# Performance work log

Hardware: AMD Instinct MI355X
Metric: run time of the kernel (lower is better)

## Reference

```python
import jax, jax.numpy as jnp
import numpy as np

N = 14           # num_wires
DEPTH = 2        # feature_map_depth; circuit applies DEPTH+1 StronglyEntanglingLayers blocks
SEL_LAYERS = 2   # params (B, 2*N*3) -> weights (B, 2, N, 3)


def _apply_1q(psi, U, w):
    # psi: (B, 2**N) complex64, U: (B,2,2) complex64, acts on wire w (wire 0 = MSB)
    B = psi.shape[0]
    psi = psi.reshape(B, 2 ** w, 2, -1)
    psi = jnp.einsum('bij,bajc->baic', U, psi)
    return psi.reshape(B, -1)


def _apply_cnot(psi, c, t):
    B = psi.shape[0]
    x = psi.reshape((B,) + (2,) * N)
    ca, ta = 1 + c, 1 + t
    a0 = jax.lax.index_in_dim(x, 0, ca, keepdims=True)
    a1 = jnp.flip(jax.lax.index_in_dim(x, 1, ca, keepdims=True), axis=ta)
    return jnp.concatenate([a0, a1], axis=ca).reshape(B, -1)


def _expz(psi, w):
    # <Z_w> = P(bit_w = 0) - P(bit_w = 1)
    B = psi.shape[0]
    p = (psi.real ** 2 + psi.imag ** 2).reshape(B, 2 ** w, 2, -1)
    return p[:, :, 0].sum(axis=(1, 2)) - p[:, :, 1].sum(axis=(1, 2))


def _rot(phi, theta, omega):
    # PennyLane Rot = RZ(omega) RY(theta) RZ(phi); returns (B,2,2) complex
    c, s = jnp.cos(theta / 2), jnp.sin(theta / 2)
    u00 = jnp.exp(-0.5j * (phi + omega)) * c
    u01 = -jnp.exp(0.5j * (phi - omega)) * s
    u10 = jnp.exp(-0.5j * (phi - omega)) * s
    u11 = jnp.exp(0.5j * (phi + omega)) * c
    return jnp.stack([jnp.stack([u00, u01], -1), jnp.stack([u10, u11], -1)], -2)


def _circuit(phases, weights):
    # phases: (B, N) float32, weights: (B, SEL_LAYERS, N, 3) float32
    B = phases.shape[0]
    psi = jnp.zeros((B, 2 ** N), jnp.complex64).at[:, 0].set(1.0)
    # AngleEmbedding (rotation='X'): RX(phi_w) on each wire
    for w in range(N):
        th = phases[:, w] / 2
        c, s = jnp.cos(th), jnp.sin(th)
        U = jnp.stack([jnp.stack([c + 0j, -1j * s], -1),
                       jnp.stack([-1j * s, c + 0j], -1)], -2)
        psi = _apply_1q(psi, U.astype(jnp.complex64), w)
    # (feature_map_depth + 1) StronglyEntanglingLayers blocks, all sharing `weights`
    for _ in range(DEPTH + 1):
        for l in range(SEL_LAYERS):
            for w in range(N):
                U = _rot(weights[:, l, w, 0], weights[:, l, w, 1], weights[:, l, w, 2])
                psi = _apply_1q(psi, U.astype(jnp.complex64), w)
            r = (l % (N - 1)) + 1  # PennyLane default ranges
            for w in range(N):
                psi = _apply_cnot(psi, w, (w + r) % N)
    return jnp.stack([_expz(psi, w) for w in range(N)], axis=1)  # (B, N)


def setup_inputs() -> dict:
    key = jax.random.key(0)
    k1, k2, k3, k4 = jax.random.split(key, 4)
    B = 512
    return {
        'state_batch': jax.random.normal(k1, (B, 2 ** N, 2), jnp.float32),
        'params': jax.random.normal(k2, (B, SEL_LAYERS * N * 3), jnp.float32),
        'head_w': jax.random.normal(k3, (1, N), jnp.float32) / np.float32(np.sqrt(N)),
        'head_b': jax.random.normal(k4, (1,), jnp.float32),
    }


def reference(state_batch, params, head_w, head_b):
    B = state_batch.shape[0]
    # torch.angle of a real tensor: pi where negative, 0 otherwise
    phases = jnp.where(state_batch.reshape(B, -1) < 0,
                       jnp.float32(np.pi), jnp.float32(0.0))[:, :N]
    weights = params.reshape(B, SEL_LAYERS, N, 3)
    qmeas = _circuit(phases, weights)            # (B, N)
    return (qmeas @ head_w.T + head_b)[:, 0]     # (B,)
```

## Files before the change

### kernel.cpp

```cpp
#include <hip/hip_runtime.h>


#define NW 14
#define NSTATE (1 << NW)
#define NTHREADS 512
#define STATE_SLOTS (NSTATE + ((NSTATE >> 6) << 1))

typedef float v2f __attribute__((ext_vector_type(2)));

__device__ __forceinline__ float2 cmul(float2 a, float2 b) {
    return make_float2(a.x * b.x - a.y * b.y, a.x * b.y + a.y * b.x);
}

__device__ __forceinline__ v2f pk_mul_bl(v2f a, v2f b) {
    v2f d; asm("v_pk_mul_f32 %0, %1, %2 op_sel:[0,0] op_sel_hi:[1,0]"
               : "=v"(d) : "v"(a), "v"(b)); return d;
}
__device__ __forceinline__ v2f pk_fma_bl(v2f a, v2f b, v2f c) {
    v2f d; asm("v_pk_fma_f32 %0, %1, %2, %3 op_sel:[0,0,0] op_sel_hi:[1,0,1]"
               : "=v"(d) : "v"(a), "v"(b), "v"(c)); return d;
}
__device__ __forceinline__ v2f pk_fma_sw(v2f a, v2f b, v2f c) {
    v2f d; asm("v_pk_fma_f32 %0, %1, %2, %3 op_sel:[1,0,0] op_sel_hi:[0,1,1]"
               : "=v"(d) : "v"(a), "v"(b), "v"(c)); return d;
}

struct RingConsts { unsigned col[2][NW]; unsigned flow[2][32]; };
constexpr RingConsts make_rc() {
    RingConsts rc{};
    for (int ri = 0; ri < 2; ++ri) {
        for (int bb = 0; bb < NW; ++bb) {
            unsigned x = 1u << bb;
            for (int w = 0; w < NW; ++w) {
                int pc = 13 - w, pt = 13 - ((w + ri + 1) % NW);
                x ^= ((x >> pc) & 1u) << pt;
            }
            rc.col[ri][bb] = x;
        }
        for (int k = 0; k < 32; ++k) {
            unsigned x = 0;
            for (int b = 0; b < 5; ++b) if ((k >> b) & 1) x ^= rc.col[ri][b];
            rc.flow[ri][k] = x;
        }
    }
    return rc;
}
constexpr RingConsts RC = make_rc();

#define GSTAGE(W) \
    const float4 g0 = G4[(W)*4+0], g1 = G4[(W)*4+1], \
                 g2 = G4[(W)*4+2], g3 = G4[(W)*4+3]; \
    const v2f U00 = (v2f){g0.x,g0.y}, V00 = (v2f){g0.z,g0.w}; \
    const v2f U01 = (v2f){g1.x,g1.y}, V01 = (v2f){g1.z,g1.w}; \
    const v2f U10 = (v2f){g2.x,g2.y}, V10 = (v2f){g2.z,g2.w}; \
    const v2f U11 = (v2f){g3.x,g3.y}, V11 = (v2f){g3.z,g3.w};

#define CBFA(X, Y) { \
    v2f n0 = pk_mul_bl(X, U00); n0 = pk_fma_sw(X, V00, n0); \
    n0 = pk_fma_bl(Y, U01, n0); n0 = pk_fma_sw(Y, V01, n0); \
    v2f n1 = pk_mul_bl(X, U10); n1 = pk_fma_sw(X, V10, n1); \
    n1 = pk_fma_bl(Y, U11, n1); n1 = pk_fma_sw(Y, V11, n1); \
    X = n0; Y = n1; }

#define FE32(M) M(0) M(1) M(2) M(3) M(4) M(5) M(6) M(7) M(8) M(9) M(10) M(11) \
    M(12) M(13) M(14) M(15) M(16) M(17) M(18) M(19) M(20) M(21) M(22) M(23) \
    M(24) M(25) M(26) M(27) M(28) M(29) M(30) M(31)

#define P4(M) M(A0,A16) M(A1,A17) M(A2,A18) M(A3,A19) M(A4,A20) M(A5,A21) M(A6,A22) M(A7,A23) \
              M(A8,A24) M(A9,A25) M(A10,A26) M(A11,A27) M(A12,A28) M(A13,A29) M(A14,A30) M(A15,A31)
#define P3(M) M(A0,A8) M(A1,A9) M(A2,A10) M(A3,A11) M(A4,A12) M(A5,A13) M(A6,A14) M(A7,A15) \
              M(A16,A24) M(A17,A25) M(A18,A26) M(A19,A27) M(A20,A28) M(A21,A29) M(A22,A30) M(A23,A31)
#define P2(M) M(A0,A4) M(A1,A5) M(A2,A6) M(A3,A7) M(A8,A12) M(A9,A13) M(A10,A14) M(A11,A15) \
              M(A16,A20) M(A17,A21) M(A18,A22) M(A19,A23) M(A24,A28) M(A25,A29) M(A26,A30) M(A27,A31)
#define P1(M) M(A0,A2) M(A1,A3) M(A4,A6) M(A5,A7) M(A8,A10) M(A9,A11) M(A12,A14) M(A13,A15) \
              M(A16,A18) M(A17,A19) M(A20,A22) M(A21,A23) M(A24,A26) M(A25,A27) M(A28,A30) M(A29,A31)
#define P0(M) M(A0,A1) M(A2,A3) M(A4,A5) M(A6,A7) M(A8,A9) M(A10,A11) M(A12,A13) M(A14,A15) \
              M(A16,A17) M(A18,A19) M(A20,A21) M(A22,A23) M(A24,A25) M(A26,A27) M(A28,A29) M(A30,A31)

template<int LO, int W0>
__device__ __forceinline__ void rot_pass5(float2* st_, const float4* G4, int t)
{
    const int base = ((t >> LO) << (LO + 5)) | (t & ((1 << LO) - 1));
    float2* pA = st_ + (base + ((base >> 6) << 1));
#define OFF(k) ((((k)) << LO) + (((((k)) << LO) >> 6) << 1))
    float2* pB = pA + OFF(16);
#define ADR(k) ((k) < 16 ? (pA + OFF(k)) : (pB + OFF((k) - 16)))
#define DECL(k) v2f A##k;
    FE32(DECL)
#undef DECL
#define LD(k) A##k = *(const v2f*)ADR(k);
    FE32(LD)
#undef LD
    { GSTAGE(W0+0) P4(CBFA) }
    { GSTAGE(W0+1) P3(CBFA) }
    { GSTAGE(W0+2) P2(CBFA) }
    { GSTAGE(W0+3) P1(CBFA) }
    { GSTAGE(W0+4) P0(CBFA) }
#define ST(k) *(v2f*)ADR(k) = A##k;
    FE32(ST)
#undef ST
#undef ADR
#undef OFF
}

#define LOW_LOAD_GATES \
    const float4* lp = (const float4*)(st_ + (32 * t + ((t >> 1) << 1))); \
    const float4 q0 = lp[0],  q1 = lp[1],  q2 = lp[2],  q3 = lp[3], \
                 q4 = lp[4],  q5 = lp[5],  q6 = lp[6],  q7 = lp[7], \
                 q8 = lp[8],  q9 = lp[9],  q10 = lp[10], q11 = lp[11], \
                 q12 = lp[12], q13 = lp[13], q14 = lp[14], q15 = lp[15]; \
    v2f A0  = (v2f){q0.x,q0.y},  A1  = (v2f){q0.z,q0.w}, \
        A2  = (v2f){q1.x,q1.y},  A3  = (v2f){q1.z,q1.w}, \
        A4  = (v2f){q2.x,q2.y},  A5  = (v2f){q2.z,q2.w}, \
        A6  = (v2f){q3.x,q3.y},  A7  = (v2f){q3.z,q3.w}, \
        A8  = (v2f){q4.x,q4.y},  A9  = (v2f){q4.z,q4.w}, \
        A10 = (v2f){q5.x,q5.y},  A11 = (v2f){q5.z,q5.w}, \
        A12 = (v2f){q6.x,q6.y},  A13 = (v2f){q6.z,q6.w}, \
        A14 = (v2f){q7.x,q7.y},  A15 = (v2f){q7.z,q7.w}, \
        A16 = (v2f){q8.x,q8.y},  A17 = (v2f){q8.z,q8.w}, \
        A18 = (v2f){q9.x,q9.y},  A19 = (v2f){q9.z,q9.w}, \
        A20 = (v2f){q10.x,q10.y}, A21 = (v2f){q10.z,q10.w}, \
        A22 = (v2f){q11.x,q11.y}, A23 = (v2f){q11.z,q11.w}, \
        A24 = (v2f){q12.x,q12.y}, A25 = (v2f){q12.z,q12.w}, \
        A26 = (v2f){q13.x,q13.y}, A27 = (v2f){q13.z,q13.w}, \
        A28 = (v2f){q14.x,q14.y}, A29 = (v2f){q14.z,q14.w}, \
        A30 = (v2f){q15.x,q15.y}, A31 = (v2f){q15.z,q15.w}; \
    { GSTAGE(10) P3(CBFA) } \
    { GSTAGE(11) P2(CBFA) } \
    { GSTAGE(12) P1(CBFA) } \
    { GSTAGE(13) P0(CBFA) }

template<int RI>
__device__ __forceinline__ void rot_low_ring5(float2* st_, const float4* G4, int t,
                                              const unsigned* lA, const unsigned* lB)
{
    LOW_LOAD_GATES
    const unsigned fb = lA[t & 31] ^ lB[t >> 5];
    __syncthreads();
#define SC(k) { const unsigned ix = fb ^ RC.flow[RI][(k)]; \
    st_[ix + ((ix >> 6) << 1)] = make_float2(A##k.x, A##k.y); }
    FE32(SC)
#undef SC
}

__device__ __forceinline__ float rot_low_meas5(float2* st_, const float4* G4, int t,
                                               const unsigned* lA, const unsigned* lB,
                                               const float* s_hw)
{
    LOW_LOAD_GATES
    const unsigned fb = lA[t & 31] ^ lB[t >> 5];
#define SGV(b) ((((fb >> b) & 1u) ? -1.f : 1.f) * s_hw[13 - (b)])
    const float sg0 = SGV(0),  sg1 = SGV(1),  sg2 = SGV(2),  sg3 = SGV(3),
                sg4 = SGV(4),  sg5 = SGV(5),  sg6 = SGV(6),  sg7 = SGV(7),
                sg8 = SGV(8),  sg9 = SGV(9),  sg10 = SGV(10), sg11 = SGV(11),
                sg12 = SGV(12), sg13 = SGV(13);
#undef SGV
    const float chiS = ((sg0 + sg1) + (sg2 + sg3)) + ((sg4 + sg5) + (sg6 + sg7))
                     + ((sg8 + sg9) + (sg10 + sg11)) + (sg12 + sg13);
#define SUBSUM(F) ( ((F)&1u?sg0:0.f) + ((F)&2u?sg1:0.f) + ((F)&4u?sg2:0.f) + ((F)&8u?sg3:0.f) \
                  + ((F)&16u?sg4:0.f) + ((F)&32u?sg5:0.f) + ((F)&64u?sg6:0.f) + ((F)&128u?sg7:0.f) \
                  + ((F)&256u?sg8:0.f) + ((F)&512u?sg9:0.f) + ((F)&1024u?sg10:0.f) + ((F)&2048u?sg11:0.f) \
                  + ((F)&4096u?sg12:0.f) + ((F)&8192u?sg13:0.f) )
    float acc = 0.f;
#define MEASK(k) { const float p2 = fmaf(A##k.x, A##k.x, A##k.y * A##k.y); \
    acc = fmaf(p2, chiS - 2.f * SUBSUM(RC.flow[1][(k)]), acc); }
    FE32(MEASK)
#undef MEASK
#undef SUBSUM
    return acc;
}

__global__ __launch_bounds__(NTHREADS, 2)
void qsim(const float* __restrict__ sb, const float* __restrict__ pr,
          const float* __restrict__ hw, const float* __restrict__ hb,
          float* __restrict__ out)
{
    __shared__ __align__(16) float2 st[STATE_SLOTS];
    __shared__ __align__(16) float4 rotc[2][NW * 4];
    __shared__ unsigned lutA[2][32], lutB[2][16];
    __shared__ float2 low_tab[32];
    __shared__ float s_hw[NW];
    __shared__ float s_red[NTHREADS / 64];
    __shared__ unsigned s_bmask;

    const int bid = blockIdx.x;
    const int t = threadIdx.x;

    if (t < 28) {
        int l = t / NW, w = t % NW;
        const float* p = pr + bid * 84 + l * 42 + w * 3;
        float phi = p[0], th = p[1], om = p[2];
        float s, cth;  __sincosf(0.5f * th, &s, &cth);
        float sa, ca, sd, cd;
        __sincosf(0.5f * (phi + om), &sa, &ca);
        __sincosf(0.5f * (phi - om), &sd, &cd);
        const float u00x = ca * cth, u00y = -sa * cth;
        const float u01x = -cd * s,  u01y = -sd * s;
        const float u10x = cd * s,   u10y = -sd * s;
        const float u11x = ca * cth, u11y = sa * cth;
        rotc[l][w*4+0] = make_float4(u00x, u00y, -u00y, u00y);
        rotc[l][w*4+1] = make_float4(u01x, u01y, -u01y, u01y);
        rotc[l][w*4+2] = make_float4(u10x, u10y, -u10y, u10y);
        rotc[l][w*4+3] = make_float4(u11x, u11y, -u11y, u11y);
    }
    if (t >= 64 && t < 128) {
        int j = t - 64, ri = j >> 5, m = j & 31;
        unsigned x = 0;
        for (int b = 0; b < 5; ++b) if ((m >> b) & 1) x ^= RC.col[ri][5 + b];
        lutA[ri][m] = x;
    }
    if (t >= 128 && t < 160) {
        int j = t - 128, ri = j >> 4, m = j & 15;
        unsigned x = 0;
        for (int b = 0; b < 4; ++b) if ((m >> b) & 1) x ^= RC.col[ri][10 + b];
        lutB[ri][m] = x;
    }
    if (t >= 160 && t < 174) s_hw[t - 160] = hw[t - 160];
    if (t == 192) {
        const float* row = sb + (size_t)bid * (NSTATE * 2);
        unsigned m = 0;
        for (int w = 0; w < NW; ++w) m |= (row[w] < 0.0f ? 1u : 0u) << (13 - w);
        s_bmask = m;
    }
    __syncthreads();
    if (t < 32) {
        const unsigned bm = s_bmask;
        float2 v = make_float2(1.f, 0.f);
#pragma unroll
        for (int b = 0; b < 5; ++b) {
            int w = 13 - b, kb = (t >> b) & 1, cb = (bm >> b) & 1;
            float4 e = rotc[0][w*4 + kb*2 + cb];
            v = cmul(v, make_float2(e.x, e.y));
        }
        low_tab[t] = v;
    }
    __syncthreads();

    {
        const unsigned bm = s_bmask;
        float2 ph = make_float2(1.f, 0.f);
#pragma unroll
        for (int w = 0; w < 9; ++w) {
            int v = (t >> (8 - w)) & 1;
            int bw = (bm >> (13 - w)) & 1;
            float4 e = rotc[0][w*4 + v*2 + bw];
            ph = cmul(ph, make_float2(e.x, e.y));
        }
        const unsigned fb = lutA[0][t & 31] ^ lutB[0][t >> 5];
#define INITK(k) { const unsigned ix = fb ^ RC.flow[0][(k)]; \
    const float2 lt = low_tab[(k)]; \
    st[ix + ((ix >> 6) << 1)] = cmul(ph, lt); }
        FE32(INITK)
#undef INITK
    }
    __syncthreads();

#pragma unroll 1
    for (int rep = 0; rep < 4; ++rep) {
        const int l = (rep & 1) ? 0 : 1;
        const float4* G4 = &rotc[l][0];
        rot_pass5<9, 0>(st, G4, t); __syncthreads();
        rot_pass5<4, 5>(st, G4, t); __syncthreads();
        if (l) rot_low_ring5<1>(st, G4, t, lutA[1], lutB[1]);
        else   rot_low_ring5<0>(st, G4, t, lutA[0], lutB[0]);
        __syncthreads();
    }
    rot_pass5<9, 0>(st, &rotc[1][0], t); __syncthreads();
    rot_pass5<4, 5>(st, &rotc[1][0], t); __syncthreads();
    float acc = rot_low_meas5(st, &rotc[1][0], t, lutA[1], lutB[1], s_hw);

    for (int off = 32; off > 0; off >>= 1) acc += __shfl_down(acc, off);
    if ((t & 63) == 0) s_red[t >> 6] = acc;
    __syncthreads();
    if (t == 0) {
        float tot = 0.f;
#pragma unroll
        for (int i = 0; i < NTHREADS / 64; ++i) tot += s_red[i];
        out[bid] = tot + hb[0];
    }
}

extern "C" void kernel_launch(void* const* d_in, const int* in_sizes, int n_in,
                              void* d_out, int out_size, void* d_ws, size_t ws_size,
                              hipStream_t stream)
{
    const float* sb = (const float*)d_in[0];
    const float* pr = (const float*)d_in[1];
    const float* hw = (const float*)d_in[2];
    const float* hb = (const float*)d_in[3];
    float* out = (float*)d_out;
    const int B = in_sizes[1] / 84;
    qsim<<<B, NTHREADS, 0, stream>>>(sb, pr, hw, hb, out);
}
```

Measured before the change: 196.6 us.

## Restructure gate passes into four 4-qubit stages with wave-local sync and 1024 threads

Doubles the block to 1024 threads, each holding 16 amplitudes instead of 32. The per-layer gate application is reorganised into stages A/B/C/D. Stages A, B and C are arranged so each wave touches only its own slice of shared memory, which lets a waitcnt stand in for two block barriers. This cuts barriers per layer and register pressure per thread, but it depends on the wave-local data ownership being correct and adds an extra LDS round-trip stage.

Measured after the change: 201.6 us. +2.6%, slower.

```diff
diff --git a/kernel.cpp b/kernel.cpp
--- a/kernel.cpp
+++ b/kernel.cpp
@@ -3,13 +3,16 @@
 
 #define NW 14
 #define NSTATE (1 << NW)
-#define NTHREADS 512
+#define NTHREADS 1024
 #define STATE_SLOTS (NSTATE + ((NSTATE >> 6) << 1))
 
 typedef float v2f __attribute__((ext_vector_type(2)));
 
 __device__ __forceinline__ float2 cmul(float2 a, float2 b) {
     return make_float2(a.x * b.x - a.y * b.y, a.x * b.y + a.y * b.x);
+}
+__device__ __forceinline__ void wavewait() {
+    asm volatile("s_waitcnt lgkmcnt(0)" ::: "memory");
 }
 
 __device__ __forceinline__ v2f pk_mul_bl(v2f a, v2f b) {
@@ -25,7 +28,7 @@
                : "=v"(d) : "v"(a), "v"(b), "v"(c)); return d;
 }
 
-struct RingConsts { unsigned col[2][NW]; unsigned flow[2][32]; };
+struct RingConsts { unsigned col[2][NW]; unsigned flowD[2][16]; };
 constexpr RingConsts make_rc() {
     RingConsts rc{};
     for (int ri = 0; ri < 2; ++ri) {
@@ -37,10 +40,10 @@
             }
             rc.col[ri][bb] = x;
         }
-        for (int k = 0; k < 32; ++k) {
+        for (int k = 0; k < 16; ++k) {
             unsigned x = 0;
-            for (int b = 0; b < 5; ++b) if ((k >> b) & 1) x ^= rc.col[ri][b];
-            rc.flow[ri][k] = x;
+            for (int j = 0; j < 4; ++j) if ((k >> j) & 1) x ^= rc.col[ri][10 + j];
+            rc.flowD[ri][k] = x;
         }
     }
     return rc;
@@ -62,53 +65,15 @@
     n1 = pk_fma_bl(Y, U11, n1); n1 = pk_fma_sw(Y, V11, n1); \
     X = n0; Y = n1; }
 
-#define FE32(M) M(0) M(1) M(2) M(3) M(4) M(5) M(6) M(7) M(8) M(9) M(10) M(11) \
-    M(12) M(13) M(14) M(15) M(16) M(17) M(18) M(19) M(20) M(21) M(22) M(23) \
-    M(24) M(25) M(26) M(27) M(28) M(29) M(30) M(31)
-
-#define P4(M) M(A0,A16) M(A1,A17) M(A2,A18) M(A3,A19) M(A4,A20) M(A5,A21) M(A6,A22) M(A7,A23) \
-              M(A8,A24) M(A9,A25) M(A10,A26) M(A11,A27) M(A12,A28) M(A13,A29) M(A14,A30) M(A15,A31)
-#define P3(M) M(A0,A8) M(A1,A9) M(A2,A10) M(A3,A11) M(A4,A12) M(A5,A13) M(A6,A14) M(A7,A15) \
-              M(A16,A24) M(A17,A25) M(A18,A26) M(A19,A27) M(A20,A28) M(A21,A29) M(A22,A30) M(A23,A31)
-#define P2(M) M(A0,A4) M(A1,A5) M(A2,A6) M(A3,A7) M(A8,A12) M(A9,A13) M(A10,A14) M(A11,A15) \
-              M(A16,A20) M(A17,A21) M(A18,A22) M(A19,A23) M(A24,A28) M(A25,A29) M(A26,A30) M(A27,A31)
-#define P1(M) M(A0,A2) M(A1,A3) M(A4,A6) M(A5,A7) M(A8,A10) M(A9,A11) M(A12,A14) M(A13,A15) \
-              M(A16,A18) M(A17,A19) M(A20,A22) M(A21,A23) M(A24,A26) M(A25,A27) M(A28,A30) M(A29,A31)
-#define P0(M) M(A0,A1) M(A2,A3) M(A4,A5) M(A6,A7) M(A8,A9) M(A10,A11) M(A12,A13) M(A14,A15) \
-              M(A16,A17) M(A18,A19) M(A20,A21) M(A22,A23) M(A24,A25) M(A26,A27) M(A28,A29) M(A30,A31)
-
-template<int LO, int W0>
-__device__ __forceinline__ void rot_pass5(float2* st_, const float4* G4, int t)
-{
-    const int base = ((t >> LO) << (LO + 5)) | (t & ((1 << LO) - 1));
-    float2* pA = st_ + (base + ((base >> 6) << 1));
-#define OFF(k) ((((k)) << LO) + (((((k)) << LO) >> 6) << 1))
-    float2* pB = pA + OFF(16);
-#define ADR(k) ((k) < 16 ? (pA + OFF(k)) : (pB + OFF((k) - 16)))
-#define DECL(k) v2f A##k;
-    FE32(DECL)
-#undef DECL
-#define LD(k) A##k = *(const v2f*)ADR(k);
-    FE32(LD)
-#undef LD
-    { GSTAGE(W0+0) P4(CBFA) }
-    { GSTAGE(W0+1) P3(CBFA) }
-    { GSTAGE(W0+2) P2(CBFA) }
-    { GSTAGE(W0+3) P1(CBFA) }
-    { GSTAGE(W0+4) P0(CBFA) }
-#define ST(k) *(v2f*)ADR(k) = A##k;
-    FE32(ST)
-#undef ST
-#undef ADR
-#undef OFF
-}
-
-#define LOW_LOAD_GATES \
-    const float4* lp = (const float4*)(st_ + (32 * t + ((t >> 1) << 1))); \
-    const float4 q0 = lp[0],  q1 = lp[1],  q2 = lp[2],  q3 = lp[3], \
-                 q4 = lp[4],  q5 = lp[5],  q6 = lp[6],  q7 = lp[7], \
-                 q8 = lp[8],  q9 = lp[9],  q10 = lp[10], q11 = lp[11], \
-                 q12 = lp[12], q13 = lp[13], q14 = lp[14], q15 = lp[15]; \
+#define FE16(M) M(0) M(1) M(2) M(3) M(4) M(5) M(6) M(7) M(8) M(9) M(10) M(11) \
+    M(12) M(13) M(14) M(15)
+
+#define Q3(M) M(A0,A8) M(A1,A9) M(A2,A10) M(A3,A11) M(A4,A12) M(A5,A13) M(A6,A14) M(A7,A15)
+#define Q2(M) M(A0,A4) M(A1,A5) M(A2,A6) M(A3,A7) M(A8,A12) M(A9,A13) M(A10,A14) M(A11,A15)
+#define Q1(M) M(A0,A2) M(A1,A3) M(A4,A6) M(A5,A7) M(A8,A10) M(A9,A11) M(A12,A14) M(A13,A15)
+#define Q0(M) M(A0,A1) M(A2,A3) M(A4,A5) M(A6,A7) M(A8,A9) M(A10,A11) M(A12,A13) M(A14,A15)
+
+#define UNPACK8Q \
     v2f A0  = (v2f){q0.x,q0.y},  A1  = (v2f){q0.z,q0.w}, \
         A2  = (v2f){q1.x,q1.y},  A3  = (v2f){q1.z,q1.w}, \
         A4  = (v2f){q2.x,q2.y},  A5  = (v2f){q2.z,q2.w}, \
@@ -116,39 +81,96 @@
         A8  = (v2f){q4.x,q4.y},  A9  = (v2f){q4.z,q4.w}, \
         A10 = (v2f){q5.x,q5.y},  A11 = (v2f){q5.z,q5.w}, \
         A12 = (v2f){q6.x,q6.y},  A13 = (v2f){q6.z,q6.w}, \
-        A14 = (v2f){q7.x,q7.y},  A15 = (v2f){q7.z,q7.w}, \
-        A16 = (v2f){q8.x,q8.y},  A17 = (v2f){q8.z,q8.w}, \
-        A18 = (v2f){q9.x,q9.y},  A19 = (v2f){q9.z,q9.w}, \
-        A20 = (v2f){q10.x,q10.y}, A21 = (v2f){q10.z,q10.w}, \
-        A22 = (v2f){q11.x,q11.y}, A23 = (v2f){q11.z,q11.w}, \
-        A24 = (v2f){q12.x,q12.y}, A25 = (v2f){q12.z,q12.w}, \
-        A26 = (v2f){q13.x,q13.y}, A27 = (v2f){q13.z,q13.w}, \
-        A28 = (v2f){q14.x,q14.y}, A29 = (v2f){q14.z,q14.w}, \
-        A30 = (v2f){q15.x,q15.y}, A31 = (v2f){q15.z,q15.w}; \
-    { GSTAGE(10) P3(CBFA) } \
-    { GSTAGE(11) P2(CBFA) } \
-    { GSTAGE(12) P1(CBFA) } \
-    { GSTAGE(13) P0(CBFA) }
+        A14 = (v2f){q7.x,q7.y},  A15 = (v2f){q7.z,q7.w};
+
+__device__ __forceinline__ void stageA(float2* st_, const float4* G4, int t)
+{
+    const int sb = (t << 4) + ((t >> 2) << 1);
+    float4* lp = (float4*)(st_ + sb);
+    const float4 q0 = lp[0], q1 = lp[1], q2 = lp[2], q3 = lp[3],
+                 q4 = lp[4], q5 = lp[5], q6 = lp[6], q7 = lp[7];
+    UNPACK8Q
+    { GSTAGE(13) Q0(CBFA) }
+    { GSTAGE(12) Q1(CBFA) }
+    { GSTAGE(11) Q2(CBFA) }
+    { GSTAGE(10) Q3(CBFA) }
+    lp[0] = make_float4(A0.x,A0.y,A1.x,A1.y);   lp[1] = make_float4(A2.x,A2.y,A3.x,A3.y);
+    lp[2] = make_float4(A4.x,A4.y,A5.x,A5.y);   lp[3] = make_float4(A6.x,A6.y,A7.x,A7.y);
+    lp[4] = make_float4(A8.x,A8.y,A9.x,A9.y);   lp[5] = make_float4(A10.x,A10.y,A11.x,A11.y);
+    lp[6] = make_float4(A12.x,A12.y,A13.x,A13.y); lp[7] = make_float4(A14.x,A14.y,A15.x,A15.y);
+}
+
+__device__ __forceinline__ void stageB(float2* st_, const float4* G4, int t)
+{
+    const int base = (t & 15) | (((t >> 4) & 3) << 8) | ((t >> 6) << 10);
+    float2* p = st_ + (base + ((base >> 6) << 1));
+#define OFFB(k) (16*(k) + (((k) >> 2) << 1))
+#define LDB(k) v2f A##k = *(const v2f*)(p + OFFB(k));
+    FE16(LDB)
+#undef LDB
+    { GSTAGE(9) Q0(CBFA) }
+    { GSTAGE(8) Q1(CBFA) }
+    { GSTAGE(7) Q2(CBFA) }
+    { GSTAGE(6) Q3(CBFA) }
+#define STB(k) *(v2f*)(p + OFFB(k)) = A##k;
+    FE16(STB)
+#undef STB
+#undef OFFB
+}
+
+__device__ __forceinline__ void stageC(float2* st_, const float4* G4, int t)
+{
+    const int base = ((t >> 6) << 10) | ((t & 63) << 2);
+    float2* p = st_ + (base + ((base >> 6) << 1));
+    float4* c0 = (float4*)(p);
+    float4* c1 = (float4*)(p + 264);
+    float4* c2 = (float4*)(p + 528);
+    float4* c3 = (float4*)(p + 792);
+    const float4 q0 = c0[0], q1 = c0[1], q2 = c1[0], q3 = c1[1],
+                 q4 = c2[0], q5 = c2[1], q6 = c3[0], q7 = c3[1];
+    UNPACK8Q
+    { GSTAGE(5) Q2(CBFA) }
+    { GSTAGE(4) Q3(CBFA) }
+    c0[0] = make_float4(A0.x,A0.y,A1.x,A1.y);   c0[1] = make_float4(A2.x,A2.y,A3.x,A3.y);
+    c1[0] = make_float4(A4.x,A4.y,A5.x,A5.y);   c1[1] = make_float4(A6.x,A6.y,A7.x,A7.y);
+    c2[0] = make_float4(A8.x,A8.y,A9.x,A9.y);   c2[1] = make_float4(A10.x,A10.y,A11.x,A11.y);
+    c3[0] = make_float4(A12.x,A12.y,A13.x,A13.y); c3[1] = make_float4(A14.x,A14.y,A15.x,A15.y);
+}
+
+#define D_LOAD_GATES \
+    float2* p = st_ + (t + ((t >> 6) << 1)); \
+    v2f A0  = *(const v2f*)(p),            A1  = *(const v2f*)(p + 1056), \
+        A2  = *(const v2f*)(p + 2*1056),   A3  = *(const v2f*)(p + 3*1056), \
+        A4  = *(const v2f*)(p + 4*1056),   A5  = *(const v2f*)(p + 5*1056), \
+        A6  = *(const v2f*)(p + 6*1056),   A7  = *(const v2f*)(p + 7*1056), \
+        A8  = *(const v2f*)(p + 8*1056),   A9  = *(const v2f*)(p + 9*1056), \
+        A10 = *(const v2f*)(p + 10*1056),  A11 = *(const v2f*)(p + 11*1056), \
+        A12 = *(const v2f*)(p + 12*1056),  A13 = *(const v2f*)(p + 13*1056), \
+        A14 = *(const v2f*)(p + 14*1056),  A15 = *(const v2f*)(p + 15*1056); \
+    { GSTAGE(3) Q0(CBFA) } \
+    { GSTAGE(2) Q1(CBFA) } \
+    { GSTAGE(1) Q2(CBFA) } \
+    { GSTAGE(0) Q3(CBFA) }
 
 template<int RI>
-__device__ __forceinline__ void rot_low_ring5(float2* st_, const float4* G4, int t,
-                                              const unsigned* lA, const unsigned* lB)
-{
-    LOW_LOAD_GATES
-    const unsigned fb = lA[t & 31] ^ lB[t >> 5];
-    __syncthreads();
-#define SC(k) { const unsigned ix = fb ^ RC.flow[RI][(k)]; \
+__device__ __forceinline__ void stageD_ring(float2* st_, const float4* G4, int t,
+                                            const unsigned* lA, const unsigned* lB)
+{
+    D_LOAD_GATES
+    const unsigned fb = lA[t & 31] ^ lB[(t >> 5) & 31];
+    __syncthreads();
+#define SC(k) { const unsigned ix = fb ^ RC.flowD[RI][(k)]; \
     st_[ix + ((ix >> 6) << 1)] = make_float2(A##k.x, A##k.y); }
-    FE32(SC)
+    FE16(SC)
 #undef SC
 }
 
-__device__ __forceinline__ float rot_low_meas5(float2* st_, const float4* G4, int t,
-                                               const unsigned* lA, const unsigned* lB,
-                                               const float* s_hw)
-{
-    LOW_LOAD_GATES
-    const unsigned fb = lA[t & 31] ^ lB[t >> 5];
+__device__ __forceinline__ float stageD_meas(float2* st_, const float4* G4, int t,
+                                             const unsigned* lA, const unsigned* lB,
+                                             const float* s_hw)
+{
+    D_LOAD_GATES
+    const unsigned fb = lA[t & 31] ^ lB[(t >> 5) & 31];
 #define SGV(b) ((((fb >> b) & 1u) ? -1.f : 1.f) * s_hw[13 - (b)])
     const float sg0 = SGV(0),  sg1 = SGV(1),  sg2 = SGV(2),  sg3 = SGV(3),
                 sg4 = SGV(4),  sg5 = SGV(5),  sg6 = SGV(6),  sg7 = SGV(7),
@@ -163,22 +185,22 @@
                   + ((F)&4096u?sg12:0.f) + ((F)&8192u?sg13:0.f) )
     float acc = 0.f;
 #define MEASK(k) { const float p2 = fmaf(A##k.x, A##k.x, A##k.y * A##k.y); \
-    acc = fmaf(p2, chiS - 2.f * SUBSUM(RC.flow[1][(k)]), acc); }
-    FE32(MEASK)
+    acc = fmaf(p2, chiS - 2.f * SUBSUM(RC.flowD[1][(k)]), acc); }
+    FE16(MEASK)
 #undef MEASK
 #undef SUBSUM
     return acc;
 }
 
-__global__ __launch_bounds__(NTHREADS, 2)
+__global__ __launch_bounds__(NTHREADS, 4)
 void qsim(const float* __restrict__ sb, const float* __restrict__ pr,
           const float* __restrict__ hw, const float* __restrict__ hb,
           float* __restrict__ out)
 {
     __shared__ __align__(16) float2 st[STATE_SLOTS];
     __shared__ __align__(16) float4 rotc[2][NW * 4];
-    __shared__ unsigned lutA[2][32], lutB[2][16];
-    __shared__ float2 low_tab[32];
+    __shared__ unsigned lutA[2][32], lutB[2][32];
+    __shared__ float2 tab16[16];
     __shared__ float s_hw[NW];
     __shared__ float s_red[NTHREADS / 64];
     __shared__ unsigned s_bmask;
@@ -206,33 +228,33 @@
     if (t >= 64 && t < 128) {
         int j = t - 64, ri = j >> 5, m = j & 31;
         unsigned x = 0;
+        for (int b = 0; b < 5; ++b) if ((m >> b) & 1) x ^= RC.col[ri][b];
+        lutA[ri][m] = x;
+    }
+    if (t >= 128 && t < 192) {
+        int j = t - 128, ri = j >> 5, m = j & 31;
+        unsigned x = 0;
         for (int b = 0; b < 5; ++b) if ((m >> b) & 1) x ^= RC.col[ri][5 + b];
-        lutA[ri][m] = x;
-    }
-    if (t >= 128 && t < 160) {
-        int j = t - 128, ri = j >> 4, m = j & 15;
-        unsigned x = 0;
-        for (int b = 0; b < 4; ++b) if ((m >> b) & 1) x ^= RC.col[ri][10 + b];
         lutB[ri][m] = x;
     }
-    if (t >= 160 && t < 174) s_hw[t - 160] = hw[t - 160];
-    if (t == 192) {
+    if (t >= 192 && t < 206) s_hw[t - 192] = hw[t - 192];
+    if (t == 224) {
         const float* row = sb + (size_t)bid * (NSTATE * 2);
         unsigned m = 0;
         for (int w = 0; w < NW; ++w) m |= (row[w] < 0.0f ? 1u : 0u) << (13 - w);
         s_bmask = m;
     }
     __syncthreads();
-    if (t < 32) {
+    if (t < 16) {
         const unsigned bm = s_bmask;
         float2 v = make_float2(1.f, 0.f);
 #pragma unroll
-        for (int b = 0; b < 5; ++b) {
-            int w = 13 - b, kb = (t >> b) & 1, cb = (bm >> b) & 1;
+        for (int j = 0; j < 4; ++j) {
+            int w = 3 - j, kb = (t >> j) & 1, cb = (bm >> (10 + j)) & 1;
             float4 e = rotc[0][w*4 + kb*2 + cb];
             v = cmul(v, make_float2(e.x, e.y));
         }
-        low_tab[t] = v;
+        tab16[t] = v;
     }
     __syncthreads();
 
@@ -240,17 +262,15 @@
         const unsigned bm = s_bmask;
         float2 ph = make_float2(1.f, 0.f);
 #pragma unroll
-        for (int w = 0; w < 9; ++w) {
-            int v = (t >> (8 - w)) & 1;
-            int bw = (bm >> (13 - w)) & 1;
-            float4 e = rotc[0][w*4 + v*2 + bw];
+        for (int b = 0; b < 10; ++b) {
+            int w = 13 - b, kb = (t >> b) & 1, cb = (bm >> b) & 1;
+            float4 e = rotc[0][w*4 + kb*2 + cb];
             ph = cmul(ph, make_float2(e.x, e.y));
         }
-        const unsigned fb = lutA[0][t & 31] ^ lutB[0][t >> 5];
-#define INITK(k) { const unsigned ix = fb ^ RC.flow[0][(k)]; \
-    const float2 lt = low_tab[(k)]; \
-    st[ix + ((ix >> 6) << 1)] = cmul(ph, lt); }
-        FE32(INITK)
+        const unsigned fb = lutA[0][t & 31] ^ lutB[0][(t >> 5) & 31];
+#define INITK(k) { const unsigned ix = fb ^ RC.flowD[0][(k)]; \
+    st[ix + ((ix >> 6) << 1)] = cmul(ph, tab16[(k)]); }
+        FE16(INITK)
 #undef INITK
     }
     __syncthreads();
@@ -259,15 +279,19 @@
     for (int rep = 0; rep < 4; ++rep) {
         const int l = (rep & 1) ? 0 : 1;
         const float4* G4 = &rotc[l][0];
-        rot_pass5<9, 0>(st, G4, t); __syncthreads();
-        rot_pass5<4, 5>(st, G4, t); __syncthreads();
-        if (l) rot_low_ring5<1>(st, G4, t, lutA[1], lutB[1]);
-        else   rot_low_ring5<0>(st, G4, t, lutA[0], lutB[0]);
+        stageA(st, G4, t); wavewait();
+        stageB(st, G4, t); wavewait();
+        stageC(st, G4, t);
         __syncthreads();
-    }
-    rot_pass5<9, 0>(st, &rotc[1][0], t); __syncthreads();
-    rot_pass5<4, 5>(st, &rotc[1][0], t); __syncthreads();
-    float acc = rot_low_meas5(st, &rotc[1][0], t, lutA[1], lutB[1], s_hw);
+        if (l) stageD_ring<1>(st, G4, t, lutA[1], lutB[1]);
+        else   stageD_ring<0>(st, G4, t, lutA[0], lutB[0]);
+        __syncthreads();
+    }
+    stageA(st, &rotc[1][0], t); wavewait();
+    stageB(st, &rotc[1][0], t); wavewait();
+    stageC(st, &rotc[1][0], t);
+    __syncthreads();
+    float acc = stageD_meas(st, &rotc[1][0], t, lutA[1], lutB[1], s_hw);
 
     for (int off = 32; off > 0; off >>= 1) acc += __shfl_down(acc, off);
     if ((t & 63) == 0) s_red[t >> 6] = acc;
```
